# Performance work log

Measured on AMD Instinct MI355X. Metric: run time of the kernel, lower is better.

Reference implementation:

```python
import jax, jax.numpy as jnp
import numpy as np

C = 256

def _conv1x1(x, w, b):
    # x: [B,C,H,W], w: [O,I], b: [O]  (1x1 conv == pointwise GEMM over channels)
    return jnp.einsum('oi,bihw->bohw', w, x) + b[None, :, None, None]

def setup_inputs() -> dict:
    key = jax.random.key(0)
    ks = jax.random.split(key, 9)
    s = 1.0 / np.sqrt(C)
    x = jax.random.normal(ks[0], (16, C, 64, 64), dtype=jnp.float32)
    wf = jax.random.uniform(ks[1], (C, C), jnp.float32, -s, s)
    bf = jax.random.uniform(ks[2], (C,), jnp.float32, -s, s)
    wg = jax.random.uniform(ks[3], (C, C), jnp.float32, -s, s)
    bg = jax.random.uniform(ks[4], (C,), jnp.float32, -s, s)
    wh = jax.random.uniform(ks[5], (C, C), jnp.float32, -s, s)
    bh = jax.random.uniform(ks[6], (C,), jnp.float32, -s, s)
    wv = jax.random.uniform(ks[7], (C, C), jnp.float32, -s, s)
    bv = jax.random.uniform(ks[8], (C,), jnp.float32, -s, s)
    return {"x": x, "wf": wf, "bf": bf, "wg": wg, "bg": bg,
            "wh": wh, "bh": bh, "wv": wv, "bv": bv}

def reference(x, wf, bf, wg, bg, wh, bh, wv, bv):
    fx = _conv1x1(x, wf, bf)              # [B,C,H,W]
    gx = _conv1x1(x, wg, bg)              # [B,C,H,W]
    # scores: fx^T @ gx over spatial H -> [B,C,W,W]
    scores = jnp.einsum('bchw,bchv->bcwv', fx, gx)
    attn = jax.nn.softmax(scores, axis=-1)  # softmax over last W dim
    hx = _conv1x1(x, wh, bh)              # [B,C,H,W]
    out = jnp.einsum('bchw,bcwv->bchv', hx, attn)  # hx @ attn -> [B,C,H,W]
    return _conv1x1(out, wv, bv)
```

## Files before the change

### kernel.cpp

```cpp
#include <hip/hip_runtime.h>
#include <math.h>

#define CH  256
#define SPA 4096
#define BB  16
#define PLANE 16777216

typedef _Float16 f16x8 __attribute__((ext_vector_type(8)));
typedef _Float16 f16x4 __attribute__((ext_vector_type(4)));
typedef float    f32x4 __attribute__((ext_vector_type(4)));

__device__ __forceinline__ void gload16(const void* g, void* l) {
    __builtin_amdgcn_global_load_lds(
        (const __attribute__((address_space(1))) unsigned int*)g,
        (__attribute__((address_space(3))) unsigned int*)l, 16, 0, 0);
}

__global__ __launch_bounds__(256) void xpose_kernel(
    const float* __restrict__ src, _Float16* __restrict__ dst)
{
    __shared__ float T[64][65];
    const int t  = threadIdx.x;
    const int b  = blockIdx.x >> 8;
    const int st = (blockIdx.x >> 2) & 63;
    const int rt = blockIdx.x & 3;
    const int s0 = st << 6, r0 = rt << 6;

    #pragma unroll
    for (int p = 0; p < 4; ++p) {
        int k = (t >> 4) + (p << 4);
        float4 v = *(const float4*)(src + (((size_t)((b << 8) + r0 + k)) << 12)
                                        + s0 + ((t & 15) << 2));
        T[k][((t & 15) << 2) + 0] = v.x;
        T[k][((t & 15) << 2) + 1] = v.y;
        T[k][((t & 15) << 2) + 2] = v.z;
        T[k][((t & 15) << 2) + 3] = v.w;
    }
    __syncthreads();

    const int s  = t >> 2;
    const int kg = (t & 3) << 4;
    const size_t obase = (((size_t)((b << 12) + s0 + s)) << 8) + r0 + kg;

    f16x8 h0, h1;
    #pragma unroll
    for (int i = 0; i < 16; ++i) {
        _Float16 hv = (_Float16)T[kg + i][s];
        if (i < 8) h0[i] = hv; else h1[i - 8] = hv;
    }
    *(f16x8*)(dst + obase)     = h0;
    *(f16x8*)(dst + obase + 8) = h1;
}

__global__ __launch_bounds__(256) void cpose_kernel(
    const _Float16* __restrict__ src, _Float16* __restrict__ dst)
{
    __shared__ _Float16 T[64][68];
    const int t  = threadIdx.x;
    const int b  = blockIdx.x >> 8;
    const int st = (blockIdx.x >> 2) & 63;
    const int ct = blockIdx.x & 3;
    const int s0 = st << 6, c0 = ct << 6;

    #pragma unroll
    for (int p = 0; p < 4; ++p) {
        int fi = (p << 8) + t;
        int r = fi >> 4, s4 = (fi & 15) << 2;
        f16x4 v = *(const f16x4*)(src + (((size_t)((b << 8) + c0 + r)) << 12) + s0 + s4);
        *(f16x4*)&T[r][s4] = v;
    }
    __syncthreads();

    const int s  = t >> 2;
    const int cg = (t & 3) << 4;
    f16x8 h0, h1;
    #pragma unroll
    for (int i = 0; i < 16; ++i) {
        _Float16 hv = T[cg + i][s];
        if (i < 8) h0[i] = hv; else h1[i - 8] = hv;
    }
    const size_t obase = (((size_t)((b << 12) + s0 + s)) << 8) + c0 + cg;
    *(f16x8*)(dst + obase)     = h0;
    *(f16x8*)(dst + obase + 8) = h1;
}

__global__ __launch_bounds__(256) void wcvt_kernel(
    const float* __restrict__ w0, const float* __restrict__ w1,
    const float* __restrict__ w2, const float* __restrict__ w3,
    _Float16* __restrict__ dst)
{
    const int idx = blockIdx.x * 256 + threadIdx.x;
    dst[idx]             = (_Float16)w0[idx];
    dst[65536 + idx]     = (_Float16)w1[idx];
    dst[131072 + idx]    = (_Float16)w2[idx];
    dst[196608 + idx]    = (_Float16)w3[idx];
}

template<bool OUTF16>
__global__ __launch_bounds__(256) void gemm16_kernel(
    const _Float16* __restrict__ xT, const _Float16* __restrict__ wc,
    const float* __restrict__ bias0, const float* __restrict__ bias1,
    const float* __restrict__ bias2, void* __restrict__ outp)
{
    __shared__ _Float16 S[8192];
    _Float16* sA = S;
    _Float16* sB = S + 4096;

    const int m = blockIdx.y;
    const _Float16* wp = wc + m * 65536;
    const float* bias = (m == 0) ? bias0 : ((m == 1) ? bias1 : bias2);

    const int tid = threadIdx.x;
    const int w = tid >> 6, lane = tid & 63, quad = lane >> 4, li = lane & 15;
    const int wx = w & 1, wy = w >> 1;
    const int ot    = blockIdx.x & 1;
    const int stile = (blockIdx.x >> 1) & 31;
    const int b     = blockIdx.x >> 6;
    const int s0 = stile << 7, o0 = ot << 7;

    f32x4 acc[4][4];
    #pragma unroll
    for (int t2 = 0; t2 < 4; ++t2)
        #pragma unroll
        for (int u = 0; u < 4; ++u) acc[t2][u] = (f32x4){0.f, 0.f, 0.f, 0.f};

    const int rr = lane >> 2, cc = (lane & 3) << 3;

    for (int kb = 0; kb < CH; kb += 32) {
        __syncthreads();
        #pragma unroll
        for (int j = 0; j < 32; j += 16) {
            const int r = (w << 5) + j + rr;
            const size_t ga = (((size_t)((b << 12) + s0 + r)) << 8) + kb + cc;
            const size_t gb = ((size_t)(o0 + r) << 8) + kb + cc;
            const int lo_ = ((w << 5) + j) * 32 + lane * 8;
            gload16(xT + ga, sA + lo_);
            gload16(wp + gb, sB + lo_);
        }
        __syncthreads();

        f16x8 a[4], bfr[4];
        #pragma unroll
        for (int t2 = 0; t2 < 4; ++t2) {
            a[t2]   = *(const f16x8*)(sA + ((wy << 6) + (t2 << 4) + li) * 32 + (quad << 3));
            bfr[t2] = *(const f16x8*)(sB + ((wx << 6) + (t2 << 4) + li) * 32 + (quad << 3));
        }
        #pragma unroll
        for (int t2 = 0; t2 < 4; ++t2)
            #pragma unroll
            for (int u = 0; u < 4; ++u)
                acc[t2][u] = __builtin_amdgcn_mfma_f32_16x16x32_f16(a[t2], bfr[u], acc[t2][u], 0, 0, 0);
    }

    #pragma unroll
    for (int u = 0; u < 4; ++u) {
        const int o = o0 + (wx << 6) + (u << 4) + li;
        const float bz = bias[o];
        #pragma unroll
        for (int t2 = 0; t2 < 4; ++t2) {
            const int s = s0 + (wy << 6) + (t2 << 4) + (quad << 2);
            const size_t off = (((size_t)((b << 8) + o)) << 12) + s;
            f32x4 v = acc[t2][u];
            if (OUTF16) {
                _Float16* ob = (_Float16*)outp + (size_t)m * PLANE;
                f16x4 pv;
                pv[0] = (_Float16)(v[0] + bz); pv[1] = (_Float16)(v[1] + bz);
                pv[2] = (_Float16)(v[2] + bz); pv[3] = (_Float16)(v[3] + bz);
                *(f16x4*)(ob + off) = pv;
            } else {
                float* of = (float*)outp;
                float4 pv = {v[0] + bz, v[1] + bz, v[2] + bz, v[3] + bz};
                *(float4*)(of + off) = pv;
            }
        }
    }
}

__global__ __launch_bounds__(256) void attn_mfma_kernel(
    const _Float16* __restrict__ fx, const _Float16* __restrict__ gx,
    const _Float16* __restrict__ hx, _Float16* __restrict__ ob)
{
    __shared__ short lds_s[27136];
    _Float16* L = (_Float16*)lds_s;
    float* Sff = (float*)(lds_s + 18432);
    const int FT = 0, GT = 4608, HM = 9216, PT = 13824;
    const int FR = 18432, GR = 13824;

    const int t = threadIdx.x;
    const int wave = t >> 6, lane = t & 63, q = lane >> 4, li = lane & 15;
    const int bc = blockIdx.x;
    const _Float16* Fp = fx + (size_t)bc * SPA;
    const _Float16* Gp = gx + (size_t)bc * SPA;
    const _Float16* Hp = hx + (size_t)bc * SPA;
    _Float16* Op = ob + (size_t)bc * SPA;

    #pragma unroll
    for (int p = 0; p < 2; ++p) {
        int ci = t + (p << 8);
        int h = ci >> 3, w8 = (ci & 7) << 3;
        f16x8 f  = *(const f16x8*)(Fp + h * 64 + w8);
        f16x8 g  = *(const f16x8*)(Gp + h * 64 + w8);
        f16x8 hh = *(const f16x8*)(Hp + h * 64 + w8);
        *(f16x8*)&L[FR + h * 72 + w8] = f;
        *(f16x8*)&L[GR + h * 72 + w8] = g;
        *(f16x8*)&L[HM + h * 72 + w8] = hh;
    }
    __syncthreads();

    {
        const int src = (wave < 2) ? FR : GR;
        const int dst = (wave < 2) ? FT : GT;
        const int mtb = (wave & 1) << 1;
        f16x8 id0, id1;
        #pragma unroll
        for (int j = 0; j < 8; ++j) {
            id0[j] = (_Float16)(((q << 3) + j == li)      ? 1.0f : 0.0f);
            id1[j] = (_Float16)(((q << 3) + j == li + 16) ? 1.0f : 0.0f);
        }
        #pragma unroll
        for (int mi = 0; mi < 2; ++mi) {
            const int mt = mtb + mi;
            f16x8 a0 = *(const f16x8*)&L[src + (mt * 16 + li) * 72 + (q << 3)];
            f16x8 a1 = *(const f16x8*)&L[src + (mt * 16 + li) * 72 + 32 + (q << 3)];
            #pragma unroll
            for (int nt = 0; nt < 4; ++nt) {
                f32x4 d = {0.f, 0.f, 0.f, 0.f};
                d = __builtin_amdgcn_mfma_f32_16x16x32_f16(
                        (nt < 2) ? a0 : a1, (nt & 1) ? id1 : id0, d, 0, 0, 0);
                f16x4 e;
                e[0] = (_Float16)d[0]; e[1] = (_Float16)d[1];
                e[2] = (_Float16)d[2]; e[3] = (_Float16)d[3];
                *(f16x4*)&L[dst + (nt * 16 + li) * 72 + mt * 16 + (q << 2)] = e;
            }
        }
    }
    __syncthreads();

    {
        f16x8 a0 = *(const f16x8*)&L[FT + (wave * 16 + li) * 72 + (q << 3)];
        f16x8 a1 = *(const f16x8*)&L[FT + (wave * 16 + li) * 72 + 32 + (q << 3)];
        f32x4 s_[4];
        #pragma unroll
        for (int nt = 0; nt < 4; ++nt) {
            f16x8 b0 = *(const f16x8*)&L[GT + (nt * 16 + li) * 72 + (q << 3)];
            f16x8 b1 = *(const f16x8*)&L[GT + (nt * 16 + li) * 72 + 32 + (q << 3)];
            f32x4 acc = {0.f, 0.f, 0.f, 0.f};
            acc = __builtin_amdgcn_mfma_f32_16x16x32_f16(a0, b0, acc, 0, 0, 0);
            acc = __builtin_amdgcn_mfma_f32_16x16x32_f16(a1, b1, acc, 0, 0, 0);
            s_[nt] = acc;
        }
        #pragma unroll
        for (int nt = 0; nt < 4; ++nt)
            #pragma unroll
            for (int r = 0; r < 4; ++r)
                Sff[(wave * 16 + (q << 2) + r) * 68 + nt * 16 + li] = s_[nt][r];
    }
    __syncthreads();

    {
        const int row = t >> 2, c0s = (t & 3) << 4;
        float e[16];
        float mx = -1e30f;
        #pragma unroll
        for (int i = 0; i < 16; ++i) {
            e[i] = Sff[row * 68 + c0s + i];
            mx = fmaxf(mx, e[i]);
        }
        mx = fmaxf(mx, __shfl_xor(mx, 1));
        mx = fmaxf(mx, __shfl_xor(mx, 2));
        float sm = 0.f;
        #pragma unroll
        for (int i = 0; i < 16; ++i) { e[i] = __expf(e[i] - mx); sm += e[i]; }
        sm += __shfl_xor(sm, 1);
        sm += __shfl_xor(sm, 2);
        const float ri = 1.f / sm;
        #pragma unroll
        for (int i = 0; i < 16; ++i) {
            const int v = c0s + i;
            const int col = row ^ (((v >> 3) & 7) << 3);
            L[PT + v * 72 + col] = (_Float16)(e[i] * ri);
        }
    }
    __syncthreads();

    {
        f16x8 a0 = *(const f16x8*)&L[HM + (wave * 16 + li) * 72 + (q << 3)];
        f16x8 a1 = *(const f16x8*)&L[HM + (wave * 16 + li) * 72 + 32 + (q << 3)];
        #pragma unroll
        for (int nt = 0; nt < 4; ++nt) {
            const int v  = nt * 16 + li;
            const int sw = ((v >> 3) & 7) << 3;
            f16x8 b0 = *(const f16x8*)&L[PT + v * 72 + ((q << 3) ^ sw)];
            f16x8 b1 = *(const f16x8*)&L[PT + v * 72 + ((32 + (q << 3)) ^ sw)];
            f32x4 acc = {0.f, 0.f, 0.f, 0.f};
            acc = __builtin_amdgcn_mfma_f32_16x16x32_f16(a0, b0, acc, 0, 0, 0);
            acc = __builtin_amdgcn_mfma_f32_16x16x32_f16(a1, b1, acc, 0, 0, 0);
            #pragma unroll
            for (int r = 0; r < 4; ++r)
                Op[(wave * 16 + (q << 2) + r) * 64 + v] = (_Float16)acc[r];
        }
    }
}

extern "C" void kernel_launch(void* const* d_in, const int* in_sizes, int n_in,
                              void* d_out, int out_size, void* d_ws, size_t ws_size,
                              hipStream_t stream)
{
    const float* x  = (const float*)d_in[0];
    const float* wf = (const float*)d_in[1];
    const float* bf = (const float*)d_in[2];
    const float* wg = (const float*)d_in[3];
    const float* bg = (const float*)d_in[4];
    const float* wh = (const float*)d_in[5];
    const float* bh = (const float*)d_in[6];
    const float* wv = (const float*)d_in[7];
    const float* bv = (const float*)d_in[8];

    char* base = (char*)d_ws;
    const size_t MB = 1ull << 20;
    _Float16* xT  = (_Float16*)base;
    _Float16* fxb = (_Float16*)(base + 32 * MB);
    _Float16* gxb = (_Float16*)(base + 64 * MB);
    _Float16* hxb = (_Float16*)(base + 96 * MB);
    _Float16* ob  = (_Float16*)(base + 128 * MB);
    _Float16* obT = (_Float16*)base;
    _Float16* wc  = (_Float16*)(base + 160 * MB);

    dim3 blk(256);
    xpose_kernel<<<4096, blk, 0, stream>>>(x, xT);
    wcvt_kernel<<<256, blk, 0, stream>>>(wf, wg, wh, wv, wc);

    gemm16_kernel<true><<<dim3(1024, 3), blk, 0, stream>>>(
        xT, wc, bf, bg, bh, fxb);

    attn_mfma_kernel<<<4096, blk, 0, stream>>>(fxb, gxb, hxb, ob);

    cpose_kernel<<<4096, blk, 0, stream>>>(ob, obT);

    gemm16_kernel<false><<<dim3(1024, 1), blk, 0, stream>>>(
        obT, wc + 196608, bv, bv, bv, d_out);
}
```

Baseline: 256.0 us.

## Compute softmax in MFMA registers and interleave projection GEMM block order

The attention kernel now computes the row softmax directly on the MFMA accumulator registers, using cross-lane shuffles for max and sum. It writes normalized probabilities straight into the swizzled P tile, removing the fp32 score staging buffer in LDS and one barrier. LDS footprint shrinks, which may allow more resident blocks per CU. The QKV projection GEMM also switches to a 1D grid where consecutive blocks cycle through the three weight matrices, so blocks reading the same activation tile run close together and can share it in cache.

```diff
diff --git a/kernel.cpp b/kernel.cpp
--- a/kernel.cpp
+++ b/kernel.cpp
@@ -96,7 +96,7 @@
     dst[196608 + idx]    = (_Float16)w3[idx];
 }
 
-template<bool OUTF16>
+template<int NM, bool OUTF16>
 __global__ __launch_bounds__(256) void gemm16_kernel(
     const _Float16* __restrict__ xT, const _Float16* __restrict__ wc,
     const float* __restrict__ bias0, const float* __restrict__ bias1,
@@ -106,16 +106,18 @@
     _Float16* sA = S;
     _Float16* sB = S + 4096;
 
-    const int m = blockIdx.y;
+    int m, r_;
+    if (NM == 3) { m = blockIdx.x % 3; r_ = blockIdx.x / 3; }
+    else         { m = 0;              r_ = blockIdx.x; }
     const _Float16* wp = wc + m * 65536;
     const float* bias = (m == 0) ? bias0 : ((m == 1) ? bias1 : bias2);
 
     const int tid = threadIdx.x;
     const int w = tid >> 6, lane = tid & 63, quad = lane >> 4, li = lane & 15;
     const int wx = w & 1, wy = w >> 1;
-    const int ot    = blockIdx.x & 1;
-    const int stile = (blockIdx.x >> 1) & 31;
-    const int b     = blockIdx.x >> 6;
+    const int ot    = r_ & 1;
+    const int stile = (r_ >> 1) & 31;
+    const int b     = r_ >> 6;
     const int s0 = stile << 7, o0 = ot << 7;
 
     f32x4 acc[4][4];
@@ -180,11 +182,10 @@
     const _Float16* __restrict__ fx, const _Float16* __restrict__ gx,
     const _Float16* __restrict__ hx, _Float16* __restrict__ ob)
 {
-    __shared__ short lds_s[27136];
-    _Float16* L = (_Float16*)lds_s;
-    float* Sff = (float*)(lds_s + 18432);
-    const int FT = 0, GT = 4608, HM = 9216, PT = 13824;
-    const int FR = 18432, GR = 13824;
+    __shared__ _Float16 L[23040];
+    const int FT = 0, GT = 4608, HM = 9216;
+    const int FR = 13824, GR = 18432;
+    const int PT = 13824;
 
     const int t = threadIdx.x;
     const int wave = t >> 6, lane = t & 63, q = lane >> 4, li = lane & 15;
@@ -198,12 +199,9 @@
     for (int p = 0; p < 2; ++p) {
         int ci = t + (p << 8);
         int h = ci >> 3, w8 = (ci & 7) << 3;
-        f16x8 f  = *(const f16x8*)(Fp + h * 64 + w8);
-        f16x8 g  = *(const f16x8*)(Gp + h * 64 + w8);
-        f16x8 hh = *(const f16x8*)(Hp + h * 64 + w8);
-        *(f16x8*)&L[FR + h * 72 + w8] = f;
-        *(f16x8*)&L[GR + h * 72 + w8] = g;
-        *(f16x8*)&L[HM + h * 72 + w8] = hh;
+        *(f16x8*)&L[FR + h * 72 + w8] = *(const f16x8*)(Fp + h * 64 + w8);
+        *(f16x8*)&L[GR + h * 72 + w8] = *(const f16x8*)(Gp + h * 64 + w8);
+        *(f16x8*)&L[HM + h * 72 + w8] = *(const f16x8*)(Hp + h * 64 + w8);
     }
     __syncthreads();
 
@@ -249,36 +247,39 @@
             acc = __builtin_amdgcn_mfma_f32_16x16x32_f16(a1, b1, acc, 0, 0, 0);
             s_[nt] = acc;
         }
+        float mx[4], sm[4];
+        #pragma unroll
+        for (int r = 0; r < 4; ++r) {
+            float m0 = fmaxf(fmaxf(s_[0][r], s_[1][r]), fmaxf(s_[2][r], s_[3][r]));
+            m0 = fmaxf(m0, __shfl_xor(m0, 1));
+            m0 = fmaxf(m0, __shfl_xor(m0, 2));
+            m0 = fmaxf(m0, __shfl_xor(m0, 4));
+            m0 = fmaxf(m0, __shfl_xor(m0, 8));
+            mx[r] = m0;
+        }
         #pragma unroll
         for (int nt = 0; nt < 4; ++nt)
             #pragma unroll
             for (int r = 0; r < 4; ++r)
-                Sff[(wave * 16 + (q << 2) + r) * 68 + nt * 16 + li] = s_[nt][r];
-    }
-    __syncthreads();
-
-    {
-        const int row = t >> 2, c0s = (t & 3) << 4;
-        float e[16];
-        float mx = -1e30f;
-        #pragma unroll
-        for (int i = 0; i < 16; ++i) {
-            e[i] = Sff[row * 68 + c0s + i];
-            mx = fmaxf(mx, e[i]);
-        }
-        mx = fmaxf(mx, __shfl_xor(mx, 1));
-        mx = fmaxf(mx, __shfl_xor(mx, 2));
-        float sm = 0.f;
-        #pragma unroll
-        for (int i = 0; i < 16; ++i) { e[i] = __expf(e[i] - mx); sm += e[i]; }
-        sm += __shfl_xor(sm, 1);
-        sm += __shfl_xor(sm, 2);
-        const float ri = 1.f / sm;
-        #pragma unroll
-        for (int i = 0; i < 16; ++i) {
-            const int v = c0s + i;
-            const int col = row ^ (((v >> 3) & 7) << 3);
-            L[PT + v * 72 + col] = (_Float16)(e[i] * ri);
+                s_[nt][r] = __expf(s_[nt][r] - mx[r]);
+        #pragma unroll
+        for (int r = 0; r < 4; ++r) {
+            float s0 = (s_[0][r] + s_[1][r]) + (s_[2][r] + s_[3][r]);
+            s0 += __shfl_xor(s0, 1);
+            s0 += __shfl_xor(s0, 2);
+            s0 += __shfl_xor(s0, 4);
+            s0 += __shfl_xor(s0, 8);
+            sm[r] = 1.f / s0;
+        }
+        #pragma unroll
+        for (int nt = 0; nt < 4; ++nt) {
+            const int v  = nt * 16 + li;
+            const int sw = ((v >> 3) & 7) << 3;
+            #pragma unroll
+            for (int r = 0; r < 4; ++r) {
+                const int w = wave * 16 + (q << 2) + r;
+                L[PT + v * 72 + (w ^ sw)] = (_Float16)(s_[nt][r] * sm[r]);
+            }
         }
     }
     __syncthreads();
@@ -330,13 +331,13 @@
     xpose_kernel<<<4096, blk, 0, stream>>>(x, xT);
     wcvt_kernel<<<256, blk, 0, stream>>>(wf, wg, wh, wv, wc);
 
-    gemm16_kernel<true><<<dim3(1024, 3), blk, 0, stream>>>(
+    gemm16_kernel<3, true><<<dim3(3072), blk, 0, stream>>>(
         xT, wc, bf, bg, bh, fxb);
 
     attn_mfma_kernel<<<4096, blk, 0, stream>>>(fxb, gxb, hxb, ob);
 
     cpose_kernel<<<4096, blk, 0, stream>>>(ob, obT);
 
-    gemm16_kernel<false><<<dim3(1024, 1), blk, 0, stream>>>(
+    gemm16_kernel<1, false><<<dim3(1024), blk, 0, stream>>>(
         obT, wc + 196608, bv, bv, bv, d_out);
 }
```

Measured after the change: 256.1 us. No clear change (+0.0%).
